# Kernel tuning notes

Measured on AMD Instinct MI355X. Metric: run time of the kernel, lower is better.

## Reference

```python
import jax, jax.numpy as jnp
import numpy as np

N = 50000      # nodes
E = 800000     # edges (before self loops)
F_IN = 256     # input features
C = 64         # out_channels per head
H = 4          # heads
NC = 3         # num_class


def setup_inputs() -> dict:
    key = jax.random.key(0)
    ks = jax.random.split(key, 11)
    s = 0.1
    return {
        "x": jax.random.normal(ks[0], (N, F_IN), jnp.float32),
        "edge_index": jax.random.randint(ks[1], (2, E), 0, N, dtype=jnp.int64),
        # conv1: in=F_IN -> H*C, concat
        "W1": jax.random.normal(ks[2], (H * C, F_IN), jnp.float32) * s,
        "as1": jax.random.normal(ks[3], (H, C), jnp.float32) * s,
        "ad1": jax.random.normal(ks[4], (H, C), jnp.float32) * s,
        "b1": jnp.zeros((H * C,), jnp.float32),
        # conv2: in=H*C -> H*C, concat
        "W2": jax.random.normal(ks[5], (H * C, H * C), jnp.float32) * s,
        "as2": jax.random.normal(ks[6], (H, C), jnp.float32) * s,
        "ad2": jax.random.normal(ks[7], (H, C), jnp.float32) * s,
        "b2": jnp.zeros((H * C,), jnp.float32),
        # conv3: in=H*C -> NC, heads averaged (concat=False)
        "W3": jax.random.normal(ks[8], (H * NC, H * C), jnp.float32) * s,
        "as3": jax.random.normal(ks[9], (H, NC), jnp.float32) * s,
        "ad3": jax.random.normal(ks[10], (H, NC), jnp.float32) * s,
        "b3": jnp.zeros((NC,), jnp.float32),
    }


def _gat_conv(x, src, dst, W, a_src, a_dst, b, concat):
    # x: [N,F]; src/dst: [E'] (self loops included); W: [H*C, F]; a_*: [H,C]
    n = x.shape[0]
    h_, c_ = a_src.shape
    h = (x @ W.T).reshape(n, h_, c_)                       # [N,H,C]
    alpha_src = (h * a_src[None]).sum(-1)                  # [N,H]
    alpha_dst = (h * a_dst[None]).sum(-1)                  # [N,H]
    e = jax.nn.leaky_relu(alpha_src[src] + alpha_dst[dst], 0.2)  # [E',H]
    # segment softmax over destination-node neighborhoods
    m = jax.ops.segment_max(e, dst, num_segments=n)        # [N,H]
    ex = jnp.exp(e - m[dst])
    den = jax.ops.segment_sum(ex, dst, num_segments=n)     # [N,H]
    alpha = ex / den[dst]                                  # [E',H]
    out = jax.ops.segment_sum(h[src] * alpha[:, :, None], dst, num_segments=n)  # [N,H,C]
    if concat:
        return out.reshape(n, h_ * c_) + b
    return out.mean(axis=1) + b


def reference(x, edge_index, W1, as1, ad1, b1, W2, as2, ad2, b2, W3, as3, ad3, b3):
    n = x.shape[0]
    loop = jnp.arange(n, dtype=edge_index.dtype)
    src = jnp.concatenate([edge_index[0], loop])  # add_self_loops=True
    dst = jnp.concatenate([edge_index[1], loop])
    x = jax.nn.elu(_gat_conv(x, src, dst, W1, as1, ad1, b1, True))
    x = jax.nn.elu(_gat_conv(x, src, dst, W2, as2, ad2, b2, True))
    x = jax.nn.elu(_gat_conv(x, src, dst, W3, as3, ad3, b3, False))
    return x
```

## Files before the change

### kernel.cpp

```cpp
#include <hip/hip_runtime.h>
#include <hip/hip_fp16.h>
#include <cstdint>
#include <cstddef>

#define NNODES 50000
#define NEDGES 800000
#define E2 (NEDGES + NNODES)
#define HC 256

typedef __attribute__((ext_vector_type(8))) short short8v;
typedef __attribute__((ext_vector_type(4))) float f32x4;


__global__ void zero_int(int* __restrict__ p, int n) {
    int i = blockIdx.x * 256 + threadIdx.x;
    if (i < n) p[i] = 0;
}

__global__ void count_deg(const int* __restrict__ ei, int* __restrict__ deg) {
    int i = blockIdx.x * 256 + threadIdx.x;
    if (i >= E2) return;
    int d = (i < NEDGES) ? ei[NEDGES + i] : (i - NEDGES);
    atomicAdd(&deg[d], 1);
}

__global__ void scan1(const int* __restrict__ deg, int* __restrict__ rp, int* __restrict__ bs) {
    __shared__ int s[256];
    int t = threadIdx.x, i = blockIdx.x * 256 + t;
    int v = (i < NNODES) ? deg[i] : 0;
    s[t] = v;
    __syncthreads();
    for (int o = 1; o < 256; o <<= 1) {
        int add = (t >= o) ? s[t - o] : 0;
        __syncthreads();
        s[t] += add;
        __syncthreads();
    }
    if (i < NNODES) rp[i] = s[t] - v;
    if (t == 255) bs[blockIdx.x] = s[255];
}

__global__ void scan2(int* __restrict__ bs, int nb) {
    __shared__ int s[256];
    int t = threadIdx.x;
    int v = (t < nb) ? bs[t] : 0;
    s[t] = v;
    __syncthreads();
    for (int o = 1; o < 256; o <<= 1) {
        int add = (t >= o) ? s[t - o] : 0;
        __syncthreads();
        s[t] += add;
        __syncthreads();
    }
    bs[t] = s[t] - v;
}

__global__ void scan3(int* __restrict__ rp, const int* __restrict__ bs, int* __restrict__ cnt) {
    int i = blockIdx.x * 256 + threadIdx.x;
    if (i < NNODES) {
        int v = rp[i] + bs[blockIdx.x];
        rp[i] = v;
        cnt[i] = v;
    }
    if (i == 0) rp[NNODES] = E2;
}

__global__ void fill_csr(const int* __restrict__ ei, int* __restrict__ cnt, int* __restrict__ csr) {
    int i = blockIdx.x * 256 + threadIdx.x;
    if (i >= E2) return;
    int s, d;
    if (i < NEDGES) { s = ei[i]; d = ei[NEDGES + i]; }
    else            { s = d = i - NEDGES; }
    int pos = atomicAdd(&cnt[d], 1);
    csr[pos] = s;
}


__device__ __forceinline__ unsigned short f2bf(float f) {
    uint32_t u = __float_as_uint(f);
    uint32_t r = (u + 0x7FFFu + ((u >> 16) & 1u)) >> 16;
    return (unsigned short)r;
}
__device__ __forceinline__ float bf2f(unsigned short h) {
    return __uint_as_float(((uint32_t)h) << 16);
}

__global__ void split_bf16(const float* __restrict__ in, unsigned short* __restrict__ hi,
                           unsigned short* __restrict__ lo, int n4) {
    int i = blockIdx.x * 256 + threadIdx.x;
    if (i >= n4) return;
    float4 v = ((const float4*)in)[i];
    unsigned short h0 = f2bf(v.x), h1 = f2bf(v.y), h2 = f2bf(v.z), h3 = f2bf(v.w);
    unsigned short l0 = f2bf(v.x - bf2f(h0));
    unsigned short l1 = f2bf(v.y - bf2f(h1));
    unsigned short l2 = f2bf(v.z - bf2f(h2));
    unsigned short l3 = f2bf(v.w - bf2f(h3));
    uint2 hp, lp;
    hp.x = (uint32_t)h0 | ((uint32_t)h1 << 16);
    hp.y = (uint32_t)h2 | ((uint32_t)h3 << 16);
    lp.x = (uint32_t)l0 | ((uint32_t)l1 << 16);
    lp.y = (uint32_t)l2 | ((uint32_t)l3 << 16);
    *(uint2*)(hi + 4 * (size_t)i) = hp;
    *(uint2*)(lo + 4 * (size_t)i) = lp;
}


__global__ __launch_bounds__(256, 2) void gemm_mfma(
    const unsigned short* __restrict__ Ah, const unsigned short* __restrict__ Al,
    const unsigned short* __restrict__ Wh, const unsigned short* __restrict__ Wl,
    float* __restrict__ out, _Float16* __restrict__ out16, int M) {
    __shared__ unsigned short sAh[128][32], sAl[128][32], sWh[128][32], sWl[128][32];
    const int t = threadIdx.x;
    const int m0 = blockIdx.x * 128, n0 = blockIdx.y * 128;
    const int lane = t & 63, w = t >> 6;
    const int wr = w >> 1, wc = w & 1;
    const int fr = lane & 15, fg = lane >> 4;

    f32x4 acc[4][4];
#pragma unroll
    for (int mi = 0; mi < 4; mi++)
#pragma unroll
        for (int ni = 0; ni < 4; ni++) acc[mi][ni] = (f32x4){0.f, 0.f, 0.f, 0.f};

    for (int kc = 0; kc < 256; kc += 32) {
#pragma unroll
        for (int i = 0; i < 2; i++) {
            int u = t + 256 * i;
            int row = u >> 2;
            int cb = (u & 3) * 8;
            int gra = m0 + row; gra = gra < M ? gra : M - 1;
            int grw = n0 + row;
            *(short8v*)&sAh[row][cb] = *(const short8v*)(Ah + (size_t)gra * HC + kc + cb);
            *(short8v*)&sAl[row][cb] = *(const short8v*)(Al + (size_t)gra * HC + kc + cb);
            *(short8v*)&sWh[row][cb] = *(const short8v*)(Wh + (size_t)grw * HC + kc + cb);
            *(short8v*)&sWl[row][cb] = *(const short8v*)(Wl + (size_t)grw * HC + kc + cb);
        }
        __syncthreads();

        short8v ah[4], al[4], bh[4], bl[4];
#pragma unroll
        for (int i = 0; i < 4; i++) {
            ah[i] = *(const short8v*)&sAh[wr * 64 + i * 16 + fr][fg * 8];
            al[i] = *(const short8v*)&sAl[wr * 64 + i * 16 + fr][fg * 8];
            bh[i] = *(const short8v*)&sWh[wc * 64 + i * 16 + fr][fg * 8];
            bl[i] = *(const short8v*)&sWl[wc * 64 + i * 16 + fr][fg * 8];
        }
#pragma unroll
        for (int mi = 0; mi < 4; mi++)
#pragma unroll
            for (int ni = 0; ni < 4; ni++) {
                acc[mi][ni] = __builtin_amdgcn_mfma_f32_16x16x32_bf16(ah[mi], bh[ni], acc[mi][ni], 0, 0, 0);
                acc[mi][ni] = __builtin_amdgcn_mfma_f32_16x16x32_bf16(ah[mi], bl[ni], acc[mi][ni], 0, 0, 0);
                acc[mi][ni] = __builtin_amdgcn_mfma_f32_16x16x32_bf16(al[mi], bh[ni], acc[mi][ni], 0, 0, 0);
            }
        __syncthreads();
    }

#pragma unroll
    for (int mi = 0; mi < 4; mi++) {
#pragma unroll
        for (int r = 0; r < 4; r++) {
            int gr = m0 + wr * 64 + mi * 16 + fg * 4 + r;
            if (gr < M) {
#pragma unroll
                for (int ni = 0; ni < 4; ni++) {
                    float v = acc[mi][ni][r];
                    size_t off = (size_t)gr * HC + n0 + wc * 64 + ni * 16 + fr;
                    out[off] = v;
                    out16[off] = (_Float16)v;
                }
            }
        }
    }
}


__global__ void alpha_hc(const float* __restrict__ h, const float* __restrict__ a_s,
                         const float* __restrict__ a_d, float* __restrict__ asrc,
                         float* __restrict__ adst) {
    int n = blockIdx.x;
    int t = threadIdx.x;
    float v = h[(size_t)n * HC + t];
    float ps = v * a_s[t];
    float pd = v * a_d[t];
    for (int o = 32; o > 0; o >>= 1) {
        ps += __shfl_xor(ps, o);
        pd += __shfl_xor(pd, o);
    }
    if ((t & 63) == 0) {
        int w = t >> 6;
        asrc[n * 4 + w] = ps;
        adst[n * 4 + w] = pd;
    }
}


#define CHUNK 512

__global__ void aggregate_hc(const _Float16* __restrict__ h16, const float* __restrict__ asrc,
                             const float* __restrict__ adst, const int* __restrict__ rp,
                             const int* __restrict__ csr, const float* __restrict__ bias,
                             float* __restrict__ y, unsigned short* __restrict__ yh,
                             unsigned short* __restrict__ yl, int flags) {
    __shared__ int   sIdx[CHUNK];
    __shared__ float sE4[CHUNK][4];
    __shared__ float sRed[4][64][4];
    __shared__ float sM[4][4], sS[4][4];
    int n = blockIdx.x;
    int t = threadIdx.x;
    int r0 = rp[n], deg = rp[n + 1] - r0;

    if (deg <= CHUNK) {
        for (int j = t; j < deg; j += 256) sIdx[j] = csr[r0 + j];
        __syncthreads();

        int hA = t & 3, jj = t >> 2;
        float adh = adst[n * 4 + hA];
        float pm = -1e30f;
        for (int j = jj; j < deg; j += 64) {
            int s = sIdx[j];
            float e = asrc[s * 4 + hA] + adh;
            e = e > 0.f ? e : 0.2f * e;
            sE4[j][hA] = e;
            pm = fmaxf(pm, e);
        }
#pragma unroll
        for (int o = 4; o <= 32; o <<= 1) pm = fmaxf(pm, __shfl_xor(pm, o));
        if ((t & 63) < 4) sM[t >> 6][t & 3] = pm;
        __syncthreads();

        float mh = fmaxf(fmaxf(sM[0][hA], sM[1][hA]), fmaxf(sM[2][hA], sM[3][hA]));
        float ps = 0.f;
        for (int j = jj; j < deg; j += 64) {
            float ex = __expf(sE4[j][hA] - mh);
            sE4[j][hA] = ex;
            ps += ex;
        }
#pragma unroll
        for (int o = 4; o <= 32; o <<= 1) ps += __shfl_xor(ps, o);
        if ((t & 63) < 4) sS[t >> 6][t & 3] = ps;
        __syncthreads();

        int wv = t >> 6, l = t & 63;
        int hh = l >> 4;
        float a0 = 0.f, a1 = 0.f, a2 = 0.f, a3 = 0.f;
        for (int j = wv; j < deg; j += 4) {
            int s = sIdx[j];
            float aw = sE4[j][hh];
            uint2 raw = *(const uint2*)(h16 + (size_t)s * HC + 4 * l);
            __half2 p0 = *(__half2*)&raw.x;
            __half2 p1 = *(__half2*)&raw.y;
            a0 = fmaf(aw, __low2float(p0), a0);
            a1 = fmaf(aw, __high2float(p0), a1);
            a2 = fmaf(aw, __low2float(p1), a2);
            a3 = fmaf(aw, __high2float(p1), a3);
        }
        sRed[wv][l][0] = a0;
        sRed[wv][l][1] = a1;
        sRed[wv][l][2] = a2;
        sRed[wv][l][3] = a3;
        __syncthreads();

        int c = t;
        float val = sRed[0][c >> 2][c & 3] + sRed[1][c >> 2][c & 3]
                  + sRed[2][c >> 2][c & 3] + sRed[3][c >> 2][c & 3];
        int ch = c >> 6;
        float ssum = sS[0][ch] + sS[1][ch] + sS[2][ch] + sS[3][ch];
        float outv = val / ssum + bias[c];
        outv = outv > 0.f ? outv : expm1f(outv);
        size_t off = (size_t)n * HC + c;
        if (flags & 1) y[off] = outv;
        if (flags & 2) {
            unsigned short hi = f2bf(outv);
            yh[off] = hi;
            yl[off] = f2bf(outv - bf2f(hi));
        }
    } else {
        int w = t >> 6, l = t & 63;
        float ad = adst[n * 4 + w];
        int hoff = (w << 6) + l;
        const _Float16* hp = h16 + hoff;
        float m = -1e30f;
        for (int j = l; j < deg; j += 64) {
            int s = csr[r0 + j];
            float e = asrc[s * 4 + w] + ad;
            e = e > 0.f ? e : 0.2f * e;
            m = fmaxf(m, e);
        }
#pragma unroll
        for (int o = 32; o > 0; o >>= 1) m = fmaxf(m, __shfl_xor(m, o));
        float acc = 0.f, ssum = 0.f;
        for (int j = 0; j < deg; j++) {
            int s = csr[r0 + j];
            float e = asrc[s * 4 + w] + ad;
            e = e > 0.f ? e : 0.2f * e;
            float a = __expf(e - m);
            ssum += a;
            acc = fmaf(a, (float)hp[(size_t)s * HC], acc);
        }
        float outv = acc / ssum + bias[hoff];
        outv = outv > 0.f ? outv : expm1f(outv);
        size_t off = (size_t)n * HC + hoff;
        if (flags & 1) y[off] = outv;
        if (flags & 2) {
            unsigned short hi = f2bf(outv);
            yh[off] = hi;
            yl[off] = f2bf(outv - bf2f(hi));
        }
    }
}


__global__ void gemm_small(const float* __restrict__ Y, const float* __restrict__ W3,
                           float* __restrict__ h3) {
    int idx = blockIdx.x * 256 + threadIdx.x;
    if (idx >= NNODES * 12) return;
    int n = idx / 12, o = idx - n * 12;
    const float4* xr = (const float4*)(Y + (size_t)n * HC);
    const float4* wr = (const float4*)(W3 + o * HC);
    float acc = 0.f;
#pragma unroll 8
    for (int k = 0; k < 64; k++) {
        float4 a = xr[k], b = wr[k];
        acc += a.x * b.x + a.y * b.y + a.z * b.z + a.w * b.w;
    }
    h3[idx] = acc;
}

__global__ void alpha3(const float* __restrict__ h3, const float* __restrict__ a_s,
                       const float* __restrict__ a_d, float* __restrict__ asrc,
                       float* __restrict__ adst) {
    int n = blockIdx.x * 256 + threadIdx.x;
    if (n >= NNODES) return;
    const float* hr = h3 + (size_t)n * 12;
    float s[4], d[4];
#pragma unroll
    for (int hh = 0; hh < 4; hh++) {
        s[hh] = hr[hh * 3] * a_s[hh * 3] + hr[hh * 3 + 1] * a_s[hh * 3 + 1] + hr[hh * 3 + 2] * a_s[hh * 3 + 2];
        d[hh] = hr[hh * 3] * a_d[hh * 3] + hr[hh * 3 + 1] * a_d[hh * 3 + 1] + hr[hh * 3 + 2] * a_d[hh * 3 + 2];
    }
    *(float4*)(asrc + n * 4) = make_float4(s[0], s[1], s[2], s[3]);
    *(float4*)(adst + n * 4) = make_float4(d[0], d[1], d[2], d[3]);
}

__global__ void aggregate3(const float* __restrict__ h3, const float* __restrict__ asrc,
                           const float* __restrict__ adst, const int* __restrict__ rp,
                           const int* __restrict__ csr, const float* __restrict__ b3,
                           float* __restrict__ out) {
    int n = blockIdx.x * 4 + (threadIdx.x >> 6);
    int l = threadIdx.x & 63;
    if (n >= NNODES) return;
    int r0 = rp[n], deg = rp[n + 1] - r0;
    float4 ad = *(const float4*)(adst + n * 4);

    float m0 = -1e30f, m1 = -1e30f, m2 = -1e30f, m3 = -1e30f;
    for (int j = l; j < deg; j += 64) {
        int s = csr[r0 + j];
        float4 a4 = *(const float4*)(asrc + s * 4);
        float e0 = a4.x + ad.x, e1 = a4.y + ad.y, e2 = a4.z + ad.z, e3 = a4.w + ad.w;
        e0 = e0 > 0.f ? e0 : 0.2f * e0;
        e1 = e1 > 0.f ? e1 : 0.2f * e1;
        e2 = e2 > 0.f ? e2 : 0.2f * e2;
        e3 = e3 > 0.f ? e3 : 0.2f * e3;
        m0 = fmaxf(m0, e0); m1 = fmaxf(m1, e1); m2 = fmaxf(m2, e2); m3 = fmaxf(m3, e3);
    }
    for (int o = 32; o > 0; o >>= 1) {
        m0 = fmaxf(m0, __shfl_xor(m0, o));
        m1 = fmaxf(m1, __shfl_xor(m1, o));
        m2 = fmaxf(m2, __shfl_xor(m2, o));
        m3 = fmaxf(m3, __shfl_xor(m3, o));
    }

    float acc[12];
#pragma unroll
    for (int k = 0; k < 12; k++) acc[k] = 0.f;
    float s0 = 0.f, s1 = 0.f, s2 = 0.f, s3 = 0.f;
    for (int j = l; j < deg; j += 64) {
        int s = csr[r0 + j];
        float4 a4 = *(const float4*)(asrc + s * 4);
        float e0 = a4.x + ad.x, e1 = a4.y + ad.y, e2 = a4.z + ad.z, e3 = a4.w + ad.w;
        e0 = e0 > 0.f ? e0 : 0.2f * e0;
        e1 = e1 > 0.f ? e1 : 0.2f * e1;
        e2 = e2 > 0.f ? e2 : 0.2f * e2;
        e3 = e3 > 0.f ? e3 : 0.2f * e3;
        float w0 = __expf(e0 - m0), w1 = __expf(e1 - m1), w2 = __expf(e2 - m2), w3 = __expf(e3 - m3);
        s0 += w0; s1 += w1; s2 += w2; s3 += w3;
        const float* hr = h3 + (size_t)s * 12;
#pragma unroll
        for (int c = 0; c < 3; c++) {
            acc[c]     += w0 * hr[c];
            acc[3 + c] += w1 * hr[3 + c];
            acc[6 + c] += w2 * hr[6 + c];
            acc[9 + c] += w3 * hr[9 + c];
        }
    }
    for (int o = 32; o > 0; o >>= 1) {
#pragma unroll
        for (int k = 0; k < 12; k++) acc[k] += __shfl_xor(acc[k], o);
        s0 += __shfl_xor(s0, o);
        s1 += __shfl_xor(s1, o);
        s2 += __shfl_xor(s2, o);
        s3 += __shfl_xor(s3, o);
    }
    if (l < 3) {
        float v = 0.25f * (acc[l] / s0 + acc[3 + l] / s1 + acc[6 + l] / s2 + acc[9 + l] / s3) + b3[l];
        v = v > 0.f ? v : expm1f(v);
        out[(size_t)n * 3 + l] = v;
    }
}


extern "C" void kernel_launch(void* const* d_in, const int* in_sizes, int n_in,
                              void* d_out, int out_size, void* d_ws, size_t ws_size,
                              hipStream_t stream) {
    (void)in_sizes; (void)n_in; (void)out_size; (void)ws_size;
    const float* x   = (const float*)d_in[0];
    const int*   ei  = (const int*)d_in[1];
    const float* W1  = (const float*)d_in[2];
    const float* as1 = (const float*)d_in[3];
    const float* ad1 = (const float*)d_in[4];
    const float* b1  = (const float*)d_in[5];
    const float* W2  = (const float*)d_in[6];
    const float* as2 = (const float*)d_in[7];
    const float* ad2 = (const float*)d_in[8];
    const float* b2  = (const float*)d_in[9];
    const float* W3  = (const float*)d_in[10];
    const float* as3 = (const float*)d_in[11];
    const float* ad3 = (const float*)d_in[12];
    const float* b3  = (const float*)d_in[13];
    float* out = (float*)d_out;

    uint8_t* p = (uint8_t*)d_ws;
    auto alloc = [&](size_t bytes) -> void* {
        void* r = (void*)p;
        p += (bytes + 255) & ~(size_t)255;
        return r;
    };
    float* bufH = (float*)alloc((size_t)NNODES * HC * 4);
    float* bufY = (float*)alloc((size_t)NNODES * HC * 4);
    float* h3   = (float*)alloc((size_t)NNODES * 12 * 4);
    float* asrc = (float*)alloc((size_t)NNODES * 4 * 4);
    float* adst = (float*)alloc((size_t)NNODES * 4 * 4);
    int* deg    = (int*)alloc((size_t)NNODES * 4);
    int* rp     = (int*)alloc((size_t)(NNODES + 1) * 4);
    int* cnt    = (int*)alloc((size_t)NNODES * 4);
    int* csr    = (int*)alloc((size_t)E2 * 4);
    int* bsums  = (int*)alloc(256 * 4);
    unsigned short* xh  = (unsigned short*)alloc((size_t)NNODES * HC * 2);
    unsigned short* xl  = (unsigned short*)alloc((size_t)NNODES * HC * 2);
    unsigned short* w1h = (unsigned short*)alloc((size_t)HC * HC * 2);
    unsigned short* w1l = (unsigned short*)alloc((size_t)HC * HC * 2);
    unsigned short* w2h = (unsigned short*)alloc((size_t)HC * HC * 2);
    unsigned short* w2l = (unsigned short*)alloc((size_t)HC * HC * 2);
    _Float16* h16 = (_Float16*)alloc((size_t)NNODES * HC * 2);

    const int NB_N = (NNODES + 255) / 256;
    const int NB_E = (E2 + 255) / 256;
    const int N4_A = NNODES * HC / 4;
    const int N4_W = HC * HC / 4;

    zero_int<<<NB_N, 256, 0, stream>>>(deg, NNODES);
    count_deg<<<NB_E, 256, 0, stream>>>(ei, deg);
    scan1<<<NB_N, 256, 0, stream>>>(deg, rp, bsums);
    scan2<<<1, 256, 0, stream>>>(bsums, NB_N);
    scan3<<<NB_N, 256, 0, stream>>>(rp, bsums, cnt);
    fill_csr<<<NB_E, 256, 0, stream>>>(ei, cnt, csr);

    dim3 ggrid((NNODES + 127) / 128, 2);

    split_bf16<<<(N4_W + 255) / 256, 256, 0, stream>>>(W1, w1h, w1l, N4_W);
    split_bf16<<<(N4_A + 255) / 256, 256, 0, stream>>>(x, xh, xl, N4_A);
    gemm_mfma<<<ggrid, 256, 0, stream>>>(xh, xl, w1h, w1l, bufH, h16, NNODES);
    alpha_hc<<<NNODES, 256, 0, stream>>>(bufH, as1, ad1, asrc, adst);
    aggregate_hc<<<NNODES, 256, 0, stream>>>(h16, asrc, adst, rp, csr, b1, bufY, xh, xl, 2);

    split_bf16<<<(N4_W + 255) / 256, 256, 0, stream>>>(W2, w2h, w2l, N4_W);
    gemm_mfma<<<ggrid, 256, 0, stream>>>(xh, xl, w2h, w2l, bufH, h16, NNODES);
    alpha_hc<<<NNODES, 256, 0, stream>>>(bufH, as2, ad2, asrc, adst);
    aggregate_hc<<<NNODES, 256, 0, stream>>>(h16, asrc, adst, rp, csr, b2, bufY, xh, xl, 1);

    gemm_small<<<(NNODES * 12 + 255) / 256, 256, 0, stream>>>(bufY, W3, h3);
    alpha3<<<NB_N, 256, 0, stream>>>(h3, as3, ad3, asrc, adst);
    aggregate3<<<(NNODES + 3) / 4, 256, 0, stream>>>(h3, asrc, adst, rp, csr, b3, out);
}
```

Before: 715.4 us.

## Drop fp32 GEMM output, use direct global-to-LDS loads, widen aggregate gathers

```diff
diff --git a/kernel.cpp b/kernel.cpp
--- a/kernel.cpp
+++ b/kernel.cpp
@@ -10,6 +10,8 @@
 
 typedef __attribute__((ext_vector_type(8))) short short8v;
 typedef __attribute__((ext_vector_type(4))) float f32x4;
+typedef const __attribute__((address_space(1))) void* gas_t;
+typedef __attribute__((address_space(3))) void* las_t;
 
 
 __global__ void zero_int(int* __restrict__ p, int n) {
@@ -108,7 +110,7 @@
 __global__ __launch_bounds__(256, 2) void gemm_mfma(
     const unsigned short* __restrict__ Ah, const unsigned short* __restrict__ Al,
     const unsigned short* __restrict__ Wh, const unsigned short* __restrict__ Wl,
-    float* __restrict__ out, _Float16* __restrict__ out16, int M) {
+    _Float16* __restrict__ out16, int M) {
     __shared__ unsigned short sAh[128][32], sAl[128][32], sWh[128][32], sWl[128][32];
     const int t = threadIdx.x;
     const int m0 = blockIdx.x * 128, n0 = blockIdx.y * 128;
@@ -116,6 +118,21 @@
     const int wr = w >> 1, wc = w & 1;
     const int fr = lane & 15, fg = lane >> 4;
 
+    const int u0 = (w * 2) * 64 + lane, u1 = (w * 2 + 1) * 64 + lane;
+    const int row0 = u0 >> 2, cb0 = (u0 & 3) * 8;
+    const int row1 = u1 >> 2, cb1 = (u1 & 3) * 8;
+    int gra0 = m0 + row0; gra0 = gra0 < M ? gra0 : M - 1;
+    int gra1 = m0 + row1; gra1 = gra1 < M ? gra1 : M - 1;
+    const int grw0 = n0 + row0, grw1 = n0 + row1;
+    unsigned short* lA0 = &sAh[(w * 2) * 16][0];
+    unsigned short* lA1 = &sAh[(w * 2 + 1) * 16][0];
+    unsigned short* lB0 = &sAl[(w * 2) * 16][0];
+    unsigned short* lB1 = &sAl[(w * 2 + 1) * 16][0];
+    unsigned short* lC0 = &sWh[(w * 2) * 16][0];
+    unsigned short* lC1 = &sWh[(w * 2 + 1) * 16][0];
+    unsigned short* lD0 = &sWl[(w * 2) * 16][0];
+    unsigned short* lD1 = &sWl[(w * 2 + 1) * 16][0];
+
     f32x4 acc[4][4];
 #pragma unroll
     for (int mi = 0; mi < 4; mi++)
@@ -123,18 +140,14 @@
         for (int ni = 0; ni < 4; ni++) acc[mi][ni] = (f32x4){0.f, 0.f, 0.f, 0.f};
 
     for (int kc = 0; kc < 256; kc += 32) {
-#pragma unroll
-        for (int i = 0; i < 2; i++) {
-            int u = t + 256 * i;
-            int row = u >> 2;
-            int cb = (u & 3) * 8;
-            int gra = m0 + row; gra = gra < M ? gra : M - 1;
-            int grw = n0 + row;
-            *(short8v*)&sAh[row][cb] = *(const short8v*)(Ah + (size_t)gra * HC + kc + cb);
-            *(short8v*)&sAl[row][cb] = *(const short8v*)(Al + (size_t)gra * HC + kc + cb);
-            *(short8v*)&sWh[row][cb] = *(const short8v*)(Wh + (size_t)grw * HC + kc + cb);
-            *(short8v*)&sWl[row][cb] = *(const short8v*)(Wl + (size_t)grw * HC + kc + cb);
-        }
+        __builtin_amdgcn_global_load_lds((gas_t)(Ah + (size_t)gra0 * HC + kc + cb0), (las_t)lA0, 16, 0, 0);
+        __builtin_amdgcn_global_load_lds((gas_t)(Ah + (size_t)gra1 * HC + kc + cb1), (las_t)lA1, 16, 0, 0);
+        __builtin_amdgcn_global_load_lds((gas_t)(Al + (size_t)gra0 * HC + kc + cb0), (las_t)lB0, 16, 0, 0);
+        __builtin_amdgcn_global_load_lds((gas_t)(Al + (size_t)gra1 * HC + kc + cb1), (las_t)lB1, 16, 0, 0);
+        __builtin_amdgcn_global_load_lds((gas_t)(Wh + (size_t)grw0 * HC + kc + cb0), (las_t)lC0, 16, 0, 0);
+        __builtin_amdgcn_global_load_lds((gas_t)(Wh + (size_t)grw1 * HC + kc + cb1), (las_t)lC1, 16, 0, 0);
+        __builtin_amdgcn_global_load_lds((gas_t)(Wl + (size_t)grw0 * HC + kc + cb0), (las_t)lD0, 16, 0, 0);
+        __builtin_amdgcn_global_load_lds((gas_t)(Wl + (size_t)grw1 * HC + kc + cb1), (las_t)lD1, 16, 0, 0);
         __syncthreads();
 
         short8v ah[4], al[4], bh[4], bl[4];
@@ -164,10 +177,7 @@
             if (gr < M) {
 #pragma unroll
                 for (int ni = 0; ni < 4; ni++) {
-                    float v = acc[mi][ni][r];
-                    size_t off = (size_t)gr * HC + n0 + wc * 64 + ni * 16 + fr;
-                    out[off] = v;
-                    out16[off] = (_Float16)v;
+                    out16[(size_t)gr * HC + n0 + wc * 64 + ni * 16 + fr] = (_Float16)acc[mi][ni][r];
                 }
             }
         }
@@ -175,12 +185,12 @@
 }
 
 
-__global__ void alpha_hc(const float* __restrict__ h, const float* __restrict__ a_s,
+__global__ void alpha_hc(const _Float16* __restrict__ h16, const float* __restrict__ a_s,
                          const float* __restrict__ a_d, float* __restrict__ asrc,
                          float* __restrict__ adst) {
     int n = blockIdx.x;
     int t = threadIdx.x;
-    float v = h[(size_t)n * HC + t];
+    float v = (float)h16[(size_t)n * HC + t];
     float ps = v * a_s[t];
     float pd = v * a_d[t];
     for (int o = 32; o > 0; o >>= 1) {
@@ -204,8 +214,8 @@
                              unsigned short* __restrict__ yl, int flags) {
     __shared__ int   sIdx[CHUNK];
     __shared__ float sE4[CHUNK][4];
-    __shared__ float sRed[4][64][4];
     __shared__ float sM[4][4], sS[4][4];
+    __shared__ float sRed[4][32][9];
     int n = blockIdx.x;
     int t = threadIdx.x;
     int r0 = rp[n], deg = rp[n + 1] - r0;
@@ -241,29 +251,31 @@
         if ((t & 63) < 4) sS[t >> 6][t & 3] = ps;
         __syncthreads();
 
-        int wv = t >> 6, l = t & 63;
-        int hh = l >> 4;
-        float a0 = 0.f, a1 = 0.f, a2 = 0.f, a3 = 0.f;
-        for (int j = wv; j < deg; j += 4) {
+        int G = t >> 5, q = t & 31, hh = q >> 3;
+        float a[8];
+#pragma unroll
+        for (int i = 0; i < 8; i++) a[i] = 0.f;
+#pragma unroll 2
+        for (int j = G; j < deg; j += 8) {
             int s = sIdx[j];
             float aw = sE4[j][hh];
-            uint2 raw = *(const uint2*)(h16 + (size_t)s * HC + 4 * l);
-            __half2 p0 = *(__half2*)&raw.x;
-            __half2 p1 = *(__half2*)&raw.y;
-            a0 = fmaf(aw, __low2float(p0), a0);
-            a1 = fmaf(aw, __high2float(p0), a1);
-            a2 = fmaf(aw, __low2float(p1), a2);
-            a3 = fmaf(aw, __high2float(p1), a3);
-        }
-        sRed[wv][l][0] = a0;
-        sRed[wv][l][1] = a1;
-        sRed[wv][l][2] = a2;
-        sRed[wv][l][3] = a3;
+            uint4 raw = *(const uint4*)(h16 + (size_t)s * HC + 8 * q);
+            const _Float16* hv = reinterpret_cast<const _Float16*>(&raw);
+#pragma unroll
+            for (int i = 0; i < 8; i++) a[i] = fmaf((float)hv[i], aw, a[i]);
+        }
+#pragma unroll
+        for (int i = 0; i < 8; i++) a[i] += __shfl_xor(a[i], 32);
+        int wv = t >> 6, l = t & 63;
+        if (l < 32) {
+#pragma unroll
+            for (int i = 0; i < 8; i++) sRed[wv][l][i] = a[i];
+        }
         __syncthreads();
 
         int c = t;
-        float val = sRed[0][c >> 2][c & 3] + sRed[1][c >> 2][c & 3]
-                  + sRed[2][c >> 2][c & 3] + sRed[3][c >> 2][c & 3];
+        float val = sRed[0][c >> 3][c & 7] + sRed[1][c >> 3][c & 7]
+                  + sRed[2][c >> 3][c & 7] + sRed[3][c >> 3][c & 7];
         int ch = c >> 6;
         float ssum = sS[0][ch] + sS[1][ch] + sS[2][ch] + sS[3][ch];
         float outv = val / ssum + bias[c];
@@ -294,9 +306,9 @@
             int s = csr[r0 + j];
             float e = asrc[s * 4 + w] + ad;
             e = e > 0.f ? e : 0.2f * e;
-            float a = __expf(e - m);
-            ssum += a;
-            acc = fmaf(a, (float)hp[(size_t)s * HC], acc);
+            float aa = __expf(e - m);
+            ssum += aa;
+            acc = fmaf(aa, (float)hp[(size_t)s * HC], acc);
         }
         float outv = acc / ssum + bias[hoff];
         outv = outv > 0.f ? outv : expm1f(outv);
@@ -436,7 +448,6 @@
         p += (bytes + 255) & ~(size_t)255;
         return r;
     };
-    float* bufH = (float*)alloc((size_t)NNODES * HC * 4);
     float* bufY = (float*)alloc((size_t)NNODES * HC * 4);
     float* h3   = (float*)alloc((size_t)NNODES * 12 * 4);
     float* asrc = (float*)alloc((size_t)NNODES * 4 * 4);
@@ -470,13 +481,13 @@
 
     split_bf16<<<(N4_W + 255) / 256, 256, 0, stream>>>(W1, w1h, w1l, N4_W);
     split_bf16<<<(N4_A + 255) / 256, 256, 0, stream>>>(x, xh, xl, N4_A);
-    gemm_mfma<<<ggrid, 256, 0, stream>>>(xh, xl, w1h, w1l, bufH, h16, NNODES);
-    alpha_hc<<<NNODES, 256, 0, stream>>>(bufH, as1, ad1, asrc, adst);
+    gemm_mfma<<<ggrid, 256, 0, stream>>>(xh, xl, w1h, w1l, h16, NNODES);
+    alpha_hc<<<NNODES, 256, 0, stream>>>(h16, as1, ad1, asrc, adst);
     aggregate_hc<<<NNODES, 256, 0, stream>>>(h16, asrc, adst, rp, csr, b1, bufY, xh, xl, 2);
 
     split_bf16<<<(N4_W + 255) / 256, 256, 0, stream>>>(W2, w2h, w2l, N4_W);
-    gemm_mfma<<<ggrid, 256, 0, stream>>>(xh, xl, w2h, w2l, bufH, h16, NNODES);
-    alpha_hc<<<NNODES, 256, 0, stream>>>(bufH, as2, ad2, asrc, adst);
+    gemm_mfma<<<ggrid, 256, 0, stream>>>(xh, xl, w2h, w2l, h16, NNODES);
+    alpha_hc<<<NNODES, 256, 0, stream>>>(h16, as2, ad2, asrc, adst);
     aggregate_hc<<<NNODES, 256, 0, stream>>>(h16, asrc, adst, rp, csr, b2, bufY, xh, xl, 1);
 
     gemm_small<<<(NNODES * 12 + 255) / 256, 256, 0, stream>>>(bufY, W3, h3);
```

Result: faster. 664.4 us (-7.1%).
